# Kernel optimization log

Measured on AMD Instinct MI355X. Metric: run time of the kernel, lower is better.

The kernel has to match this reference:

```python
import math
import jax, jax.numpy as jnp
import numpy as np

B, N, D, O, S = 16, 4096, 64, 12, 32
K_TOD, K_DOW = 8, 4
M = K_TOD + K_DOW
A = 32  # attn_dim
ALPHA = 0.1
GATE_BOUND = 1.0
TEMP = 1.0


def setup_inputs() -> dict:
    key = jax.random.key(0)
    ks = jax.random.split(key, 10)
    sc = 0.05
    return {
        "H": jax.random.normal(ks[0], (B, N, D), jnp.float32),
        "ts_out": jax.random.uniform(ks[1], (B, O, 2), jnp.float32),
        "step_emb": jax.random.normal(ks[2], (B, O, S), jnp.float32),
        "key_emb": jax.random.normal(ks[3], (M, A), jnp.float32) * sc,
        "val_emb": jax.random.normal(ks[4], (M, D), jnp.float32) * sc,
        "Wk": jax.random.normal(ks[5], (A, 2), jnp.float32) * sc,
        "Wg": jax.random.normal(ks[6], (1, 2), jnp.float32) * sc,
        "bg": jnp.zeros((1,), jnp.float32),
        "Wq": jax.random.normal(ks[7], (A, D + S), jnp.float32) * sc,
        "bq": jnp.zeros((A,), jnp.float32),
    }


def _fourier_tokens(phase, K):
    # phase: [B,O]; returns [B,O,K,2] of (sin, cos) for harmonics k=1..K
    k = jnp.arange(1, K + 1, dtype=phase.dtype)  # [K]
    ang = 2.0 * math.pi * phase[..., None] * k   # [B,O,K]
    return jnp.stack([jnp.sin(ang), jnp.cos(ang)], axis=-1)


def reference(H, ts_out, step_emb, key_emb, val_emb, Wk, Wg, bg, Wq, bq):
    tod = ts_out[..., 0]
    dow = ts_out[..., 1]
    # Fourier time tokens: [B,O,M,2]
    tok = jnp.concatenate(
        [_fourier_tokens(tod, K_TOD), _fourier_tokens(dow, K_DOW)], axis=2
    )
    # keys / gates / values over the M tokens (tiny side)
    key = jnp.einsum("bomt,at->boma", tok, Wk) + key_emb[None, None]      # [B,O,M,A]
    gate = jnp.tanh(jnp.einsum("bomt,gt->bomg", tok, Wg) + bg) * GATE_BOUND  # [B,O,M,1]
    val = gate * val_emb[None, None]                                       # [B,O,M,D]
    # query: split Linear(D+S) into H-part and step-part to avoid materializing q_in
    qh = jnp.einsum("bnd,ad->bna", H, Wq[:, :D])            # [B,N,A]
    qs = jnp.einsum("bos,as->boa", step_emb, Wq[:, D:]) + bq  # [B,O,A]
    q = qh[:, None, :, :] + qs[:, :, None, :]                # [B,O,N,A]
    scale = 1.0 / (math.sqrt(float(A)) * max(TEMP, 1e-6))
    logits = jnp.einsum("bona,boma->bonm", q, key) * scale   # [B,O,N,M]
    attn = jax.nn.softmax(logits, axis=-1)
    delta = jnp.einsum("bonm,bomd->bond", attn, val)         # [B,O,N,D]
    H_time = H[:, None, :, :] + ALPHA * delta                # [B,O,N,D]
    return (H_time, attn, gate[..., 0])
```

## Files before the change

kernel.cpp:

```cpp
#include <hip/hip_runtime.h>
#include <math.h>

#define BB 16
#define NN 4096
#define DD 64
#define OO 12
#define SS 32
#define MM 12
#define AA 32

__global__ __launch_bounds__(256, 4) void stta_kernel(
    const float* __restrict__ H, const float* __restrict__ ts_out,
    const float* __restrict__ step_emb, const float* __restrict__ key_emb,
    const float* __restrict__ val_emb, const float* __restrict__ Wk,
    const float* __restrict__ Wg, const float* __restrict__ bgp,
    const float* __restrict__ Wq, const float* __restrict__ bq,
    float* __restrict__ out)
{
    const int b = blockIdx.y;
    const int n0 = blockIdx.x * 64;
    const int tid = threadIdx.x;

    __shared__ float s_wq[32 * 64];
    __shared__ float s_ke[MM * AA];
    __shared__ float s_ve[MM * DD];
    __shared__ float s_wk0[32], s_wk1[32];
    __shared__ float s_tokS[OO * MM], s_tokC[OO * MM], s_gate[OO * MM];
    __shared__ float s_qs[OO * AA];
    __shared__ float s_c2[OO * MM];

    float* outH    = out;
    float* outAttn = out + (size_t)BB * OO * NN * DD;
    float* outGate = outAttn + (size_t)BB * OO * NN * MM;

    const float scale = 0.17677669529663687f;

    for (int i = tid; i < 32 * 64; i += 256) {
        int a = i >> 6, d = i & 63;
        s_wq[i] = Wq[a * 96 + d];
    }
    for (int i = tid; i < MM * AA; i += 256) s_ke[i] = key_emb[i];
    for (int i = tid; i < MM * DD; i += 256) s_ve[i] = val_emb[i];
    if (tid < 32) { s_wk0[tid] = Wk[tid * 2]; s_wk1[tid] = Wk[tid * 2 + 1]; }

    const float wg0 = Wg[0], wg1 = Wg[1], bg0 = bgp[0];
    for (int i = tid; i < OO * MM; i += 256) {
        int o = i / MM, m = i - o * MM;
        float phase = ts_out[(b * OO + o) * 2 + (m < 8 ? 0 : 1)];
        float k = (m < 8) ? (float)(m + 1) : (float)(m - 7);
        float ang = 6.283185307179586f * phase * k;
        float sv = sinf(ang), cv = cosf(ang);
        s_tokS[i] = sv; s_tokC[i] = cv;
        float gv = tanhf(sv * wg0 + cv * wg1 + bg0);
        s_gate[i] = gv;
        if (blockIdx.x == 0) outGate[(b * OO + o) * MM + m] = gv;
    }
    for (int e = tid; e < OO * AA; e += 256) {
        int o = e >> 5, a = e & 31;
        float acc = bq[a];
        const float* se = step_emb + (b * OO + o) * SS;
        const float* wq = Wq + a * 96 + 64;
        #pragma unroll
        for (int s = 0; s < SS; s++) acc += se[s] * wq[s];
        s_qs[e] = acc;
    }
    __syncthreads();

    for (int i = tid; i < OO * MM; i += 256) {
        int o = i / MM, m = i - o * MM;
        float S = s_tokS[i], C = s_tokC[i];
        float acc = 0.f;
        const float* qs = s_qs + o * 32;
        const float* ke = s_ke + m * 32;
        #pragma unroll
        for (int a = 0; a < 32; a++)
            acc += qs[a] * (S * s_wk0[a] + C * s_wk1[a] + ke[a]);
        s_c2[i] = acc * scale;
    }
    __syncthreads();

    const int nl = tid >> 2, g = tid & 3;
    const int n = n0 + nl;

    const float4* h4p = reinterpret_cast<const float4*>(H + ((size_t)b * NN + n) * DD + g * 16);
    float4 h40 = h4p[0], h41 = h4p[1], h42 = h4p[2], h43 = h4p[3];
    float h[16] = { h40.x,h40.y,h40.z,h40.w, h41.x,h41.y,h41.z,h41.w,
                    h42.x,h42.y,h42.z,h42.w, h43.x,h43.y,h43.z,h43.w };

    float uh = 0.f, vh = 0.f;
    float wh[12] = {0,0,0,0,0,0,0,0,0,0,0,0};
    {
        float qh[32];
        #pragma unroll
        for (int a = 0; a < 32; a++) {
            const float4* wq4 = reinterpret_cast<const float4*>(s_wq + a * 64 + g * 16);
            float4 w0 = wq4[0], w1 = wq4[1], w2 = wq4[2], w3 = wq4[3];
            qh[a] = h[0]*w0.x + h[1]*w0.y + h[2]*w0.z + h[3]*w0.w
                  + h[4]*w1.x + h[5]*w1.y + h[6]*w1.z + h[7]*w1.w
                  + h[8]*w2.x + h[9]*w2.y + h[10]*w2.z + h[11]*w2.w
                  + h[12]*w3.x + h[13]*w3.y + h[14]*w3.z + h[15]*w3.w;
        }
        #pragma unroll
        for (int a = 0; a < 32; a++) qh[a] += __shfl_xor(qh[a], 1);
        #pragma unroll
        for (int a = 0; a < 32; a++) qh[a] += __shfl_xor(qh[a], 2);

        #pragma unroll
        for (int a = 0; a < 32; a++) { uh += qh[a] * s_wk0[a]; vh += qh[a] * s_wk1[a]; }
        #pragma unroll
        for (int m = 0; m < 12; m++) {
            const float* ke = s_ke + m * 32;
            float acc = 0.f;
            #pragma unroll
            for (int a = 0; a < 32; a++) acc += qh[a] * ke[a];
            wh[m] = acc * scale;
        }
        uh *= scale; vh *= scale;
    }

    const float4* ve4 = reinterpret_cast<const float4*>(s_ve);

    for (int o = 0; o < OO; o++) {
        float lg[12], mx = -1e30f;
        #pragma unroll
        for (int m = 0; m < 12; m++) {
            int i = o * 12 + m;
            lg[m] = s_tokS[i] * uh + s_tokC[i] * vh + wh[m] + s_c2[i];
            mx = fmaxf(mx, lg[m]);
        }
        float sum = 0.f;
        #pragma unroll
        for (int m = 0; m < 12; m++) { lg[m] = __expf(lg[m] - mx); sum += lg[m]; }
        float inv = 1.f / sum;

        size_t abase = ((size_t)(b * OO + o) * NN + n) * MM;
        if (g == 0) {
            *reinterpret_cast<float4*>(outAttn + abase) =
                make_float4(lg[0]*inv, lg[1]*inv, lg[2]*inv, lg[3]*inv);
        } else if (g == 1) {
            *reinterpret_cast<float4*>(outAttn + abase + 4) =
                make_float4(lg[4]*inv, lg[5]*inv, lg[6]*inv, lg[7]*inv);
        } else if (g == 2) {
            *reinterpret_cast<float4*>(outAttn + abase + 8) =
                make_float4(lg[8]*inv, lg[9]*inv, lg[10]*inv, lg[11]*inv);
        }

        float ag[12];
        #pragma unroll
        for (int m = 0; m < 12; m++) ag[m] = lg[m] * inv * s_gate[o * 12 + m];

        size_t hbase = ((size_t)(b * OO + o) * NN + n) * DD + g * 16;
        float4* outp = reinterpret_cast<float4*>(outH + hbase);
        #pragma unroll
        for (int jj = 0; jj < 4; jj++) {
            float ax = 0.f, ay = 0.f, az = 0.f, aw = 0.f;
            #pragma unroll
            for (int m = 0; m < 12; m++) {
                float4 vv = ve4[m * 16 + g * 4 + jj];
                ax += ag[m] * vv.x; ay += ag[m] * vv.y;
                az += ag[m] * vv.z; aw += ag[m] * vv.w;
            }
            outp[jj] = make_float4(h[jj*4+0] + 0.1f*ax, h[jj*4+1] + 0.1f*ay,
                                   h[jj*4+2] + 0.1f*az, h[jj*4+3] + 0.1f*aw);
        }
    }
}

extern "C" void kernel_launch(void* const* d_in, const int* in_sizes, int n_in,
                              void* d_out, int out_size, void* d_ws, size_t ws_size,
                              hipStream_t stream) {
    const float* H        = (const float*)d_in[0];
    const float* ts_out   = (const float*)d_in[1];
    const float* step_emb = (const float*)d_in[2];
    const float* key_emb  = (const float*)d_in[3];
    const float* val_emb  = (const float*)d_in[4];
    const float* Wk       = (const float*)d_in[5];
    const float* Wg       = (const float*)d_in[6];
    const float* bg       = (const float*)d_in[7];
    const float* Wq       = (const float*)d_in[8];
    const float* bq       = (const float*)d_in[9];
    float* outp = (float*)d_out;

    dim3 grid(NN / 64, BB);
    stta_kernel<<<grid, 256, 0, stream>>>(H, ts_out, step_emb, key_emb, val_emb,
                                          Wk, Wg, bg, Wq, bq, outp);
}
```

Baseline: 294.5 us.

## Interleave per-thread D columns, use nontemporal stores, and process two outputs per iteration

```diff
diff --git a/kernel.cpp b/kernel.cpp
--- a/kernel.cpp
+++ b/kernel.cpp
@@ -8,6 +8,13 @@
 #define SS 32
 #define MM 12
 #define AA 32
+
+typedef float v4f __attribute__((ext_vector_type(4)));
+
+__device__ __forceinline__ void nt_store4(float* p, float x, float y, float z, float w) {
+    v4f v = {x, y, z, w};
+    __builtin_nontemporal_store(v, reinterpret_cast<v4f*>(p));
+}
 
 __global__ __launch_bounds__(256, 4) void stta_kernel(
     const float* __restrict__ H, const float* __restrict__ ts_out,
@@ -21,13 +28,16 @@
     const int n0 = blockIdx.x * 64;
     const int tid = threadIdx.x;
 
-    __shared__ float s_wq[32 * 64];
-    __shared__ float s_ke[MM * AA];
-    __shared__ float s_ve[MM * DD];
-    __shared__ float s_wk0[32], s_wk1[32];
-    __shared__ float s_tokS[OO * MM], s_tokC[OO * MM], s_gate[OO * MM];
-    __shared__ float s_qs[OO * AA];
-    __shared__ float s_c2[OO * MM];
+    __shared__ __align__(16) float s_wq[32 * 64];
+    __shared__ __align__(16) float s_ke[MM * AA];
+    __shared__ __align__(16) float s_ve[MM * DD];
+    __shared__ __align__(16) float s_wk0[32];
+    __shared__ __align__(16) float s_wk1[32];
+    __shared__ __align__(16) float s_tokS[OO * MM];
+    __shared__ __align__(16) float s_tokC[OO * MM];
+    __shared__ __align__(16) float s_gate[OO * MM];
+    __shared__ __align__(16) float s_qs[OO * AA];
+    __shared__ __align__(16) float s_c2[OO * MM];
 
     float* outH    = out;
     float* outAttn = out + (size_t)BB * OO * NN * DD;
@@ -35,12 +45,23 @@
 
     const float scale = 0.17677669529663687f;
 
-    for (int i = tid; i < 32 * 64; i += 256) {
-        int a = i >> 6, d = i & 63;
-        s_wq[i] = Wq[a * 96 + d];
-    }
-    for (int i = tid; i < MM * AA; i += 256) s_ke[i] = key_emb[i];
-    for (int i = tid; i < MM * DD; i += 256) s_ve[i] = val_emb[i];
+    {
+        float4* dst = reinterpret_cast<float4*>(s_wq);
+        for (int i = tid; i < 512; i += 256) {
+            int a = i >> 4, dq = i & 15;
+            dst[i] = reinterpret_cast<const float4*>(Wq + a * 96)[dq];
+        }
+    }
+    {
+        float4* dst = reinterpret_cast<float4*>(s_ke);
+        const float4* src = reinterpret_cast<const float4*>(key_emb);
+        for (int i = tid; i < (MM * AA) / 4; i += 256) dst[i] = src[i];
+    }
+    {
+        float4* dst = reinterpret_cast<float4*>(s_ve);
+        const float4* src = reinterpret_cast<const float4*>(val_emb);
+        for (int i = tid; i < (MM * DD) / 4; i += 256) dst[i] = src[i];
+    }
     if (tid < 32) { s_wk0[tid] = Wk[tid * 2]; s_wk1[tid] = Wk[tid * 2 + 1]; }
 
     const float wg0 = Wg[0], wg1 = Wg[1], bg0 = bgp[0];
@@ -82,10 +103,13 @@
     const int nl = tid >> 2, g = tid & 3;
     const int n = n0 + nl;
 
-    const float4* h4p = reinterpret_cast<const float4*>(H + ((size_t)b * NN + n) * DD + g * 16);
-    float4 h40 = h4p[0], h41 = h4p[1], h42 = h4p[2], h43 = h4p[3];
-    float h[16] = { h40.x,h40.y,h40.z,h40.w, h41.x,h41.y,h41.z,h41.w,
-                    h42.x,h42.y,h42.z,h42.w, h43.x,h43.y,h43.z,h43.w };
+    const float4* hrow = reinterpret_cast<const float4*>(H + ((size_t)b * NN + n) * DD);
+    float h[16];
+    #pragma unroll
+    for (int jj = 0; jj < 4; jj++) {
+        float4 v = hrow[g + 4 * jj];
+        h[jj*4+0] = v.x; h[jj*4+1] = v.y; h[jj*4+2] = v.z; h[jj*4+3] = v.w;
+    }
 
     float uh = 0.f, vh = 0.f;
     float wh[12] = {0,0,0,0,0,0,0,0,0,0,0,0};
@@ -93,26 +117,37 @@
         float qh[32];
         #pragma unroll
         for (int a = 0; a < 32; a++) {
-            const float4* wq4 = reinterpret_cast<const float4*>(s_wq + a * 64 + g * 16);
-            float4 w0 = wq4[0], w1 = wq4[1], w2 = wq4[2], w3 = wq4[3];
-            qh[a] = h[0]*w0.x + h[1]*w0.y + h[2]*w0.z + h[3]*w0.w
-                  + h[4]*w1.x + h[5]*w1.y + h[6]*w1.z + h[7]*w1.w
-                  + h[8]*w2.x + h[9]*w2.y + h[10]*w2.z + h[11]*w2.w
-                  + h[12]*w3.x + h[13]*w3.y + h[14]*w3.z + h[15]*w3.w;
-        }
-        #pragma unroll
-        for (int a = 0; a < 32; a++) qh[a] += __shfl_xor(qh[a], 1);
-        #pragma unroll
-        for (int a = 0; a < 32; a++) qh[a] += __shfl_xor(qh[a], 2);
-
-        #pragma unroll
-        for (int a = 0; a < 32; a++) { uh += qh[a] * s_wk0[a]; vh += qh[a] * s_wk1[a]; }
-        #pragma unroll
-        for (int m = 0; m < 12; m++) {
-            const float* ke = s_ke + m * 32;
+            const float4* wq4 = reinterpret_cast<const float4*>(s_wq + a * 64);
             float acc = 0.f;
             #pragma unroll
-            for (int a = 0; a < 32; a++) acc += qh[a] * ke[a];
+            for (int jj = 0; jj < 4; jj++) {
+                float4 w = wq4[g + 4 * jj];
+                acc += h[jj*4+0]*w.x + h[jj*4+1]*w.y + h[jj*4+2]*w.z + h[jj*4+3]*w.w;
+            }
+            qh[a] = acc;
+        }
+        #pragma unroll
+        for (int a = 0; a < 32; a++) qh[a] += __shfl_xor(qh[a], 1);
+        #pragma unroll
+        for (int a = 0; a < 32; a++) qh[a] += __shfl_xor(qh[a], 2);
+
+        const float4* k0 = reinterpret_cast<const float4*>(s_wk0);
+        const float4* k1 = reinterpret_cast<const float4*>(s_wk1);
+        #pragma unroll
+        for (int q = 0; q < 8; q++) {
+            float4 a0 = k0[q], a1 = k1[q];
+            uh += qh[q*4+0]*a0.x + qh[q*4+1]*a0.y + qh[q*4+2]*a0.z + qh[q*4+3]*a0.w;
+            vh += qh[q*4+0]*a1.x + qh[q*4+1]*a1.y + qh[q*4+2]*a1.z + qh[q*4+3]*a1.w;
+        }
+        #pragma unroll
+        for (int m = 0; m < 12; m++) {
+            const float4* ke = reinterpret_cast<const float4*>(s_ke + m * 32);
+            float acc = 0.f;
+            #pragma unroll
+            for (int q = 0; q < 8; q++) {
+                float4 k4 = ke[q];
+                acc += qh[q*4+0]*k4.x + qh[q*4+1]*k4.y + qh[q*4+2]*k4.z + qh[q*4+3]*k4.w;
+            }
             wh[m] = acc * scale;
         }
         uh *= scale; vh *= scale;
@@ -120,48 +155,85 @@
 
     const float4* ve4 = reinterpret_cast<const float4*>(s_ve);
 
-    for (int o = 0; o < OO; o++) {
-        float lg[12], mx = -1e30f;
+    for (int op = 0; op < OO; op += 2) {
+        const float4* tS  = reinterpret_cast<const float4*>(s_tokS + op * 12);
+        const float4* tC  = reinterpret_cast<const float4*>(s_tokC + op * 12);
+        const float4* tc2 = reinterpret_cast<const float4*>(s_c2   + op * 12);
+        const float4* tgt = reinterpret_cast<const float4*>(s_gate + op * 12);
+
+        float lg0[12], lg1[12];
+        #pragma unroll
+        for (int q = 0; q < 3; q++) {
+            float4 S = tS[q], C = tC[q], c = tc2[q];
+            lg0[q*4+0] = S.x*uh + C.x*vh + wh[q*4+0] + c.x;
+            lg0[q*4+1] = S.y*uh + C.y*vh + wh[q*4+1] + c.y;
+            lg0[q*4+2] = S.z*uh + C.z*vh + wh[q*4+2] + c.z;
+            lg0[q*4+3] = S.w*uh + C.w*vh + wh[q*4+3] + c.w;
+        }
+        #pragma unroll
+        for (int q = 0; q < 3; q++) {
+            float4 S = tS[3+q], C = tC[3+q], c = tc2[3+q];
+            lg1[q*4+0] = S.x*uh + C.x*vh + wh[q*4+0] + c.x;
+            lg1[q*4+1] = S.y*uh + C.y*vh + wh[q*4+1] + c.y;
+            lg1[q*4+2] = S.z*uh + C.z*vh + wh[q*4+2] + c.z;
+            lg1[q*4+3] = S.w*uh + C.w*vh + wh[q*4+3] + c.w;
+        }
+
+        float mx0 = -1e30f, mx1 = -1e30f;
+        #pragma unroll
+        for (int m = 0; m < 12; m++) { mx0 = fmaxf(mx0, lg0[m]); mx1 = fmaxf(mx1, lg1[m]); }
+        float sum0 = 0.f, sum1 = 0.f;
         #pragma unroll
         for (int m = 0; m < 12; m++) {
-            int i = o * 12 + m;
-            lg[m] = s_tokS[i] * uh + s_tokC[i] * vh + wh[m] + s_c2[i];
-            mx = fmaxf(mx, lg[m]);
-        }
-        float sum = 0.f;
-        #pragma unroll
-        for (int m = 0; m < 12; m++) { lg[m] = __expf(lg[m] - mx); sum += lg[m]; }
-        float inv = 1.f / sum;
-
-        size_t abase = ((size_t)(b * OO + o) * NN + n) * MM;
+            lg0[m] = __expf(lg0[m] - mx0); sum0 += lg0[m];
+            lg1[m] = __expf(lg1[m] - mx1); sum1 += lg1[m];
+        }
+        float inv0 = 1.f / sum0, inv1 = 1.f / sum1;
+        #pragma unroll
+        for (int m = 0; m < 12; m++) { lg0[m] *= inv0; lg1[m] *= inv1; }
+
+        size_t abase0 = ((size_t)(b * OO + op) * NN + n) * MM;
+        size_t abase1 = abase0 + (size_t)NN * MM;
         if (g == 0) {
-            *reinterpret_cast<float4*>(outAttn + abase) =
-                make_float4(lg[0]*inv, lg[1]*inv, lg[2]*inv, lg[3]*inv);
+            nt_store4(outAttn + abase0, lg0[0], lg0[1], lg0[2], lg0[3]);
+            nt_store4(outAttn + abase1, lg1[0], lg1[1], lg1[2], lg1[3]);
         } else if (g == 1) {
-            *reinterpret_cast<float4*>(outAttn + abase + 4) =
-                make_float4(lg[4]*inv, lg[5]*inv, lg[6]*inv, lg[7]*inv);
+            nt_store4(outAttn + abase0 + 4, lg0[4], lg0[5], lg0[6], lg0[7]);
+            nt_store4(outAttn + abase1 + 4, lg1[4], lg1[5], lg1[6], lg1[7]);
         } else if (g == 2) {
-            *reinterpret_cast<float4*>(outAttn + abase + 8) =
-                make_float4(lg[8]*inv, lg[9]*inv, lg[10]*inv, lg[11]*inv);
-        }
-
-        float ag[12];
-        #pragma unroll
-        for (int m = 0; m < 12; m++) ag[m] = lg[m] * inv * s_gate[o * 12 + m];
-
-        size_t hbase = ((size_t)(b * OO + o) * NN + n) * DD + g * 16;
-        float4* outp = reinterpret_cast<float4*>(outH + hbase);
+            nt_store4(outAttn + abase0 + 8, lg0[8], lg0[9], lg0[10], lg0[11]);
+            nt_store4(outAttn + abase1 + 8, lg1[8], lg1[9], lg1[10], lg1[11]);
+        }
+
+        #pragma unroll
+        for (int q = 0; q < 3; q++) {
+            float4 g0 = tgt[q], g1 = tgt[3+q];
+            lg0[q*4+0] *= g0.x; lg0[q*4+1] *= g0.y; lg0[q*4+2] *= g0.z; lg0[q*4+3] *= g0.w;
+            lg1[q*4+0] *= g1.x; lg1[q*4+1] *= g1.y; lg1[q*4+2] *= g1.z; lg1[q*4+3] *= g1.w;
+        }
+
+        size_t hbase = ((size_t)(b * OO + op) * NN + n) * DD;
+        float* outp0 = outH + hbase;
+        float* outp1 = outH + hbase + (size_t)NN * DD;
         #pragma unroll
         for (int jj = 0; jj < 4; jj++) {
-            float ax = 0.f, ay = 0.f, az = 0.f, aw = 0.f;
+            float ax0=0.f, ay0=0.f, az0=0.f, aw0=0.f;
+            float ax1=0.f, ay1=0.f, az1=0.f, aw1=0.f;
             #pragma unroll
             for (int m = 0; m < 12; m++) {
-                float4 vv = ve4[m * 16 + g * 4 + jj];
-                ax += ag[m] * vv.x; ay += ag[m] * vv.y;
-                az += ag[m] * vv.z; aw += ag[m] * vv.w;
+                float4 vv = ve4[m * 16 + g + 4 * jj];
+                ax0 += lg0[m]*vv.x; ay0 += lg0[m]*vv.y;
+                az0 += lg0[m]*vv.z; aw0 += lg0[m]*vv.w;
+                ax1 += lg1[m]*vv.x; ay1 += lg1[m]*vv.y;
+                az1 += lg1[m]*vv.z; aw1 += lg1[m]*vv.w;
             }
-            outp[jj] = make_float4(h[jj*4+0] + 0.1f*ax, h[jj*4+1] + 0.1f*ay,
-                                   h[jj*4+2] + 0.1f*az, h[jj*4+3] + 0.1f*aw);
+            int off = (g + 4 * jj) * 4;
+            nt_store4(outp0 + off,
+                      h[jj*4+0] + 0.1f*ax0, h[jj*4+1] + 0.1f*ay0,
+                      h[jj*4+2] + 0.1f*az0, h[jj*4+3] + 0.1f*aw0);
+            nt_store4(outp1 + off,
+                      h[jj*4+0] + 0.1f*ax1, h[jj*4+1] + 0.1f*ay1,
+                      h[jj*4+2] + 0.1f*az1, h[jj*4+3] + 0.1f*aw1);
         }
     }
 }
```

New measurement: 327.3 us. 11.1% more time.
